# Optimization experiments

Hardware: AMD Instinct MI355X
Metric: run time of the kernel (lower is better)

Reference implementation:

```python
import jax, jax.numpy as jnp
import numpy as np

B, N, M, Q, H, D = 1, 512, 512, 128, 8, 16
CLIP = 10.0

def _xavier(key, shape):
    # xavier_uniform over last two dims (fan_in=Q, fan_out=D per head)
    fan_in, fan_out = shape[-2], shape[-1]
    limit = float(np.sqrt(6.0 / (fan_in + fan_out)))
    return jax.random.uniform(key, shape, jnp.float32, -limit, limit)

def setup_inputs() -> dict:
    key = jax.random.key(0)
    ks = jax.random.split(key, 12)
    return {
        "x": jax.random.normal(ks[0], (B, N, Q), jnp.float32),
        "y": jax.random.normal(ks[1], (B, M, Q), jnp.float32),
        "z": jax.random.normal(ks[2], (B, N, M, Q), jnp.float32),
        "mask": jax.random.randint(ks[3], (B, N, M), 0, 2, jnp.int32),
        "lambda_x": _xavier(ks[4], (H, Q, D)),
        "lambda_y": _xavier(ks[5], (H, Q, D)),
        "lambda_z1": _xavier(ks[6], (H, Q, D)),
        "lambda_z2": _xavier(ks[7], (H, Q, D)),
        "bias_lambda_x": jnp.zeros((H, D), jnp.float32),
        "bias_lambda_y": jnp.zeros((H, D), jnp.float32),
        "theta1": _xavier(ks[8], (H, Q, D)),
        "theta2": _xavier(ks[9], (H, Q, D)),
        "bias_theta": jnp.zeros((H, D), jnp.float32),
    }

def reference(x, y, z, mask, lambda_x, lambda_y, lambda_z1, lambda_z2,
              bias_lambda_x, bias_lambda_y, theta1, theta2, bias_theta):
    head_dim = lambda_x.shape[-1]
    # node projections: [B,N,H,D] / [B,M,H,D]
    r_x = jnp.einsum('bnq,hqd->bnhd', x, lambda_x) + bias_lambda_x
    r_y = jnp.einsum('bmq,hqd->bmhd', y, lambda_y) + bias_lambda_y
    # edge projections: [B,N,M,H,D]
    r_z1 = jnp.einsum('bnmq,hqd->bnmhd', z, lambda_z1)
    r_z2 = jnp.einsum('bnmq,hqd->bnmhd', z, lambda_z2)
    # broadcast-add node + edge terms, dot over D -> scores [B,H,N,M]
    att = jnp.einsum('bnmhd,bnmhd->bhnm',
                     r_x[:, :, None, :, :] + r_z1,
                     r_y[:, None, :, :, :] + r_z2)
    att = att * (head_dim ** -0.5)
    att = CLIP * jnp.tanh(att)
    att = jnp.where(mask[:, None, :, :] == 1, -jnp.inf, att)
    # NOTE: softmax over the N (source) axis, matching torch dim=-2
    w = jax.nn.softmax(att, axis=-2)
    x_p = jnp.einsum('bnq,hqd->bnhd', x, theta1)
    r = jnp.einsum('bhnm,bnhd->bmhd', w, x_p) + bias_theta
    return jnp.einsum('bmhd,hqd->bmq', r, theta2)
```

## Files before the change

### kernel.cpp

```cpp
#include <hip/hip_runtime.h>
#include <hip/hip_bf16.h>
#include <math.h>

typedef __attribute__((ext_vector_type(8))) short short8;
typedef __attribute__((ext_vector_type(4))) float f32x4;

#define NT 8

__global__ __launch_bounds__(128) void prep_kernel(
        const float* __restrict__ x,  const float* __restrict__ y,
        const float* __restrict__ lx, const float* __restrict__ ly,
        const float* __restrict__ t1,
        const float* __restrict__ lz1, const float* __restrict__ lz2,
        const float* __restrict__ th2, const float* __restrict__ bth,
        const float* __restrict__ blx, const float* __restrict__ bly,
        __hip_bfloat16* __restrict__ Wh, __hip_bfloat16* __restrict__ Wl,
        float* __restrict__ T2, float* __restrict__ ob,
        float* __restrict__ rx, float* __restrict__ ry, float* __restrict__ xp) {
    const int bid = blockIdx.x;
    const int t = threadIdx.x;
    if (bid < 256) {
        __shared__ float rows[4][128];
        const int role = bid >> 7;
        const int n0 = (bid & 127) * 4;
        const float* in = role ? y : x;
        const int o = t, h = o >> 4, d = o & 15;
#pragma unroll
        for (int j = 0; j < 4; ++j)
            rows[j][o] = in[(n0 + j) * 128 + o];
        __syncthreads();
        if (role == 0) {
            float a[4] = {0.f, 0.f, 0.f, 0.f}, b[4] = {0.f, 0.f, 0.f, 0.f};
#pragma unroll 4
            for (int q = 0; q < 128; ++q) {
                float wa = lx[(h * 128 + q) * 16 + d];
                float wb = t1[(h * 128 + q) * 16 + d];
#pragma unroll
                for (int j = 0; j < 4; ++j) {
                    a[j] = fmaf(rows[j][q], wa, a[j]);
                    b[j] = fmaf(rows[j][q], wb, b[j]);
                }
            }
            float bx = blx[o];
#pragma unroll
            for (int j = 0; j < 4; ++j) {
                rx[(n0 + j) * 128 + o] = a[j] + bx;
                xp[(n0 + j) * 128 + o] = b[j];
            }
        } else {
            float a[4] = {0.f, 0.f, 0.f, 0.f};
#pragma unroll 4
            for (int q = 0; q < 128; ++q) {
                float wa = ly[(h * 128 + q) * 16 + d];
#pragma unroll
                for (int j = 0; j < 4; ++j)
                    a[j] = fmaf(rows[j][q], wa, a[j]);
            }
            float by = bly[o];
#pragma unroll
            for (int j = 0; j < 4; ++j)
                ry[(n0 + j) * 128 + o] = a[j] + by;
        }
    } else {
        const int idx = (bid - 256) * 128 + t;
#pragma unroll
        for (int i = idx; i < 32768; i += 16384) {
            int op = i >> 7, q = i & 127;
            int h = op >> 5, wh = (op >> 4) & 1, d = op & 15;
            float v = (wh ? lz2 : lz1)[(h * 128 + q) * 16 + d];
            __hip_bfloat16 hb = __float2bfloat16(v);
            Wh[i] = hb;
            Wl[i] = __float2bfloat16(v - __bfloat162float(hb));
        }
        {
            int o = idx >> 7, q = idx & 127;
            int h = o >> 4, d = o & 15;
            T2[idx] = th2[(h * 128 + q) * 16 + d];
        }
        if (idx < 128) {
            int q = idx;
            float s = 0.f;
#pragma unroll
            for (int h = 0; h < 8; ++h)
#pragma unroll
                for (int c = 0; c < 4; ++c) {
                    float4 a = *(const float4*)&bth[h * 16 + c * 4];
                    float4 b = *(const float4*)&th2[(h * 128 + q) * 16 + c * 4];
                    s += a.x * b.x + a.y * b.y + a.z * b.z + a.w * b.w;
                }
            ob[q] = s;
        }
    }
}

__global__ __launch_bounds__(256) void big_kernel(
        const float* __restrict__ z,
        const int* __restrict__ mask,
        const __hip_bfloat16* __restrict__ Wh,
        const __hip_bfloat16* __restrict__ Wl,
        const float* __restrict__ rx,
        const float* __restrict__ ry,
        float* __restrict__ w) {
    __shared__ short zsh[2][64 * 128];
    __shared__ short zsl[2][64 * 128];
    const int m0 = blockIdx.x * 64;
    const int n0 = blockIdx.y * NT;
    const int tid = threadIdx.x;
    const int og = tid >> 6;
    const int l  = tid & 63;
    const int lg = l >> 4;
    const int lm = l & 15;

    const int srow = tid >> 2, kseg = tid & 3;
    const float* zbase = &z[(size_t)(m0 + srow) * 128 + kseg * 32];

    float4 ryr[2][4];
#pragma unroll
    for (int p = 0; p < 2; ++p)
#pragma unroll
        for (int i = 0; i < 4; ++i)
            ryr[p][i] = *(const float4*)&ry[(size_t)(m0 + i * 16 + lm) * 128 + (og * 2 + p) * 16 + lg * 4];

    float4 zr[8];
#define LOADZ(nn)                                                         \
    {                                                                     \
        const float* p_ = zbase + (size_t)(nn) * 65536;                   \
        _Pragma("unroll")                                                 \
        for (int c_ = 0; c_ < 8; ++c_) zr[c_] = *(const float4*)&p_[c_ * 4]; \
    }

#define CONVERT_WRITE(b)                                                  \
    {                                                                     \
        _Pragma("unroll")                                                 \
        for (int c8 = 0; c8 < 4; ++c8) {                                  \
            float vv[8] = {zr[2 * c8].x, zr[2 * c8].y, zr[2 * c8].z, zr[2 * c8].w, \
                           zr[2 * c8 + 1].x, zr[2 * c8 + 1].y, zr[2 * c8 + 1].z, zr[2 * c8 + 1].w}; \
            union { short8 s; __hip_bfloat16 h[8]; } uh, ul;              \
            _Pragma("unroll")                                             \
            for (int jj = 0; jj < 8; ++jj) {                              \
                float f_ = vv[jj];                                        \
                __hip_bfloat16 hb_ = __float2bfloat16(f_);                \
                uh.h[jj] = hb_;                                           \
                ul.h[jj] = __float2bfloat16(f_ - __bfloat162float(hb_));  \
            }                                                             \
            int cw_ = (kseg * 4 + c8) ^ (srow & 7);                       \
            *(short8*)&zsh[b][srow * 128 + cw_ * 8] = uh.s;               \
            *(short8*)&zsl[b][srow * 128 + cw_ * 8] = ul.s;               \
        }                                                                 \
    }

    LOADZ(n0);
    CONVERT_WRITE(0);
    LOADZ(n0 + 1);
    __syncthreads();

    for (int t = 0; t < NT; ++t) {
        const int n = n0 + t;
        const int cur = t & 1;
        const int mk = mask[n * 512 + m0 + l];

        f32x4 acc[4][4];
#pragma unroll
        for (int i = 0; i < 4; ++i)
#pragma unroll
            for (int pj = 0; pj < 4; ++pj) acc[i][pj] = (f32x4){0.f, 0.f, 0.f, 0.f};

#pragma unroll
        for (int ks = 0; ks < 4; ++ks) {
            short8 ah[4], al[4];
#pragma unroll
            for (int i = 0; i < 4; ++i) {
                int row = i * 16 + lm;
                int cw = (ks * 4 + lg) ^ (row & 7);
                ah[i] = *(const short8*)&zsh[cur][row * 128 + cw * 8];
                al[i] = *(const short8*)&zsl[cur][row * 128 + cw * 8];
            }
#pragma unroll
            for (int pj = 0; pj < 4; ++pj) {
                size_t off = (size_t)(og * 64 + pj * 16 + lm) * 128 + ks * 32 + lg * 8;
                short8 bh = *(const short8*)&Wh[off];
                short8 bl = *(const short8*)&Wl[off];
#pragma unroll
                for (int i = 0; i < 4; ++i) {
                    acc[i][pj] = __builtin_amdgcn_mfma_f32_16x16x32_bf16(bh, ah[i], acc[i][pj], 0, 0, 0);
                    acc[i][pj] = __builtin_amdgcn_mfma_f32_16x16x32_bf16(bh, al[i], acc[i][pj], 0, 0, 0);
                    acc[i][pj] = __builtin_amdgcn_mfma_f32_16x16x32_bf16(bl, ah[i], acc[i][pj], 0, 0, 0);
                }
            }
        }

#pragma unroll
        for (int p = 0; p < 2; ++p) {
            const int h = og * 2 + p;
            float4 rxt = *(const float4*)&rx[n * 128 + h * 16 + lg * 4];
            const float rxv[4] = {rxt.x, rxt.y, rxt.z, rxt.w};
            float t4[4];
#pragma unroll
            for (int i = 0; i < 4; ++i) {
                const float ryv[4] = {ryr[p][i].x, ryr[p][i].y, ryr[p][i].z, ryr[p][i].w};
                float s = 0.f;
#pragma unroll
                for (int r = 0; r < 4; ++r)
                    s = fmaf(rxv[r] + acc[i][p * 2][r], ryv[r] + acc[i][p * 2 + 1][r], s);
                s += __shfl_xor(s, 16);
                s += __shfl_xor(s, 32);
                t4[i] = s;
            }
            float ta = (lg & 1) ? t4[1] : t4[0];
            float tb = (lg & 1) ? t4[3] : t4[2];
            float s  = (lg & 2) ? tb : ta;
            float e1 = __expf(0.5f * s);
            float wv = __expf(-20.f / (e1 + 1.f));
            if (mk == 1) wv = 0.f;
            w[((size_t)(h * 512 + n)) * 512 + m0 + l] = wv;
        }

        if (t + 1 < NT) {
            CONVERT_WRITE(cur ^ 1);
            if (t + 2 < NT) LOADZ(n0 + t + 2);
        }
        __syncthreads();
    }
#undef LOADZ
#undef CONVERT_WRITE
}

__global__ __launch_bounds__(256) void finish_kernel(
        const float* __restrict__ w,
        const float* __restrict__ xp,
        const float* __restrict__ T2,
        const float* __restrict__ ob,
        float* __restrict__ out) {
    __shared__ float xps[512][16];
    __shared__ float red[32][8][16];
    __shared__ float ssum[32][8];
    __shared__ float rrs[8][128];
    const int m0 = blockIdx.x * 8;
    const int t  = threadIdx.x;
    const int ml = t & 7, g = t >> 3;

    for (int h = 0; h < 8; ++h) {
        for (int idx = t; idx < 512 * 4; idx += 256) {
            int nn = idx >> 2, c = idx & 3;
            *(float4*)&xps[nn][c * 4] = *(const float4*)&xp[nn * 128 + h * 16 + c * 4];
        }
        __syncthreads();

        const float* col = &w[((size_t)h * 512) * 512 + m0 + ml];
        float s = 0.f;
        float racc[16];
#pragma unroll
        for (int dd = 0; dd < 16; ++dd) racc[dd] = 0.f;
        for (int nn = g * 16; nn < g * 16 + 16; ++nn) {
            float e = col[(size_t)nn * 512];
            s += e;
#pragma unroll
            for (int c = 0; c < 4; ++c) {
                float4 xv = *(const float4*)&xps[nn][c * 4];
                racc[c * 4 + 0] = fmaf(e, xv.x, racc[c * 4 + 0]);
                racc[c * 4 + 1] = fmaf(e, xv.y, racc[c * 4 + 1]);
                racc[c * 4 + 2] = fmaf(e, xv.z, racc[c * 4 + 2]);
                racc[c * 4 + 3] = fmaf(e, xv.w, racc[c * 4 + 3]);
            }
        }
        ssum[g][ml] = s;
#pragma unroll
        for (int dd = 0; dd < 16; ++dd) red[g][ml][dd] = racc[dd];
        __syncthreads();

        if (t < 128) {
            const int m = t & 7, dd = t >> 3;
            float stot = 0.f;
#pragma unroll
            for (int gg = 0; gg < 32; ++gg) stot += ssum[gg][m];
            float v = 0.f;
#pragma unroll
            for (int gg = 0; gg < 32; ++gg) v += red[gg][m][dd];
            rrs[m][h * 16 + dd] = v / stot;
        }
        __syncthreads();
    }

    {
        const int q = t & 127, mg = t >> 7;
        float acc4[4] = {0.f, 0.f, 0.f, 0.f};
        for (int o4 = 0; o4 < 32; ++o4) {
            float tv[4];
#pragma unroll
            for (int k = 0; k < 4; ++k)
                tv[k] = T2[(o4 * 4 + k) * 128 + q];
#pragma unroll
            for (int j = 0; j < 4; ++j) {
                float4 rv = *(const float4*)&rrs[mg * 4 + j][o4 * 4];
                acc4[j] = fmaf(rv.x, tv[0], acc4[j]);
                acc4[j] = fmaf(rv.y, tv[1], acc4[j]);
                acc4[j] = fmaf(rv.z, tv[2], acc4[j]);
                acc4[j] = fmaf(rv.w, tv[3], acc4[j]);
            }
        }
        float b = ob[q];
#pragma unroll
        for (int j = 0; j < 4; ++j)
            out[(m0 + mg * 4 + j) * 128 + q] = acc4[j] + b;
    }
}

extern "C" void kernel_launch(void* const* d_in, const int* in_sizes, int n_in,
                              void* d_out, int out_size, void* d_ws, size_t ws_size,
                              hipStream_t stream) {
    (void)in_sizes; (void)n_in; (void)out_size; (void)ws_size;
    const float* x   = (const float*)d_in[0];
    const float* y   = (const float*)d_in[1];
    const float* z   = (const float*)d_in[2];
    const int*  mask = (const int*)d_in[3];
    const float* lx  = (const float*)d_in[4];
    const float* ly  = (const float*)d_in[5];
    const float* lz1 = (const float*)d_in[6];
    const float* lz2 = (const float*)d_in[7];
    const float* blx = (const float*)d_in[8];
    const float* bly = (const float*)d_in[9];
    const float* t1  = (const float*)d_in[10];
    const float* t2  = (const float*)d_in[11];
    const float* bth = (const float*)d_in[12];
    float* out = (float*)d_out;

    float* ws = (float*)d_ws;
    float* rx = ws;
    float* ry = rx + 65536;
    float* xp = ry + 65536;
    __hip_bfloat16* Wh = (__hip_bfloat16*)(xp + 65536);
    __hip_bfloat16* Wl = (__hip_bfloat16*)(xp + 65536 + 16384);
    float* T2  = xp + 65536 + 32768;
    float* ob  = T2 + 16384;
    float* wbuf= ob + 128;

    prep_kernel<<<dim3(384), dim3(128), 0, stream>>>(
        x, y, lx, ly, t1, lz1, lz2, t2, bth, blx, bly,
        Wh, Wl, T2, ob, rx, ry, xp);
    big_kernel<<<dim3(8, 64), dim3(256), 0, stream>>>(z, mask, Wh, Wl, rx, ry, wbuf);
    finish_kernel<<<dim3(64), dim3(256), 0, stream>>>(wbuf, xp, T2, ob, out);
}
```

Measured before the change: 297.7 us.

## Split finish kernel across heads and single-buffer z tile in big kernel

The finish stage, which looped over all 8 heads in 64 blocks, is split into a per-head pv_kernel launched on a 64x8 grid and a separate outg_kernel that applies the output projection. This raises parallelism in the tail stage, which was badly under-occupied. The big kernel's double-buffered LDS z tile becomes single-buffered, with a sync after the MFMA loop so the next tile's conversion overlaps the epilogue. That halves LDS use and may allow more resident blocks, at the cost of an extra barrier per iteration and an extra kernel launch.

```diff
diff --git a/kernel.cpp b/kernel.cpp
--- a/kernel.cpp
+++ b/kernel.cpp
@@ -101,8 +101,8 @@
         const float* __restrict__ rx,
         const float* __restrict__ ry,
         float* __restrict__ w) {
-    __shared__ short zsh[2][64 * 128];
-    __shared__ short zsl[2][64 * 128];
+    __shared__ short zsh[64 * 128];
+    __shared__ short zsl[64 * 128];
     const int m0 = blockIdx.x * 64;
     const int n0 = blockIdx.y * NT;
     const int tid = threadIdx.x;
@@ -129,7 +129,7 @@
         for (int c_ = 0; c_ < 8; ++c_) zr[c_] = *(const float4*)&p_[c_ * 4]; \
     }
 
-#define CONVERT_WRITE(b)                                                  \
+#define CONVERT_WRITE()                                                   \
     {                                                                     \
         _Pragma("unroll")                                                 \
         for (int c8 = 0; c8 < 4; ++c8) {                                  \
@@ -144,19 +144,18 @@
                 ul.h[jj] = __float2bfloat16(f_ - __bfloat162float(hb_));  \
             }                                                             \
             int cw_ = (kseg * 4 + c8) ^ (srow & 7);                       \
-            *(short8*)&zsh[b][srow * 128 + cw_ * 8] = uh.s;               \
-            *(short8*)&zsl[b][srow * 128 + cw_ * 8] = ul.s;               \
+            *(short8*)&zsh[srow * 128 + cw_ * 8] = uh.s;                  \
+            *(short8*)&zsl[srow * 128 + cw_ * 8] = ul.s;                  \
         }                                                                 \
     }
 
     LOADZ(n0);
-    CONVERT_WRITE(0);
+    CONVERT_WRITE();
     LOADZ(n0 + 1);
     __syncthreads();
 
     for (int t = 0; t < NT; ++t) {
         const int n = n0 + t;
-        const int cur = t & 1;
         const int mk = mask[n * 512 + m0 + l];
 
         f32x4 acc[4][4];
@@ -172,8 +171,8 @@
             for (int i = 0; i < 4; ++i) {
                 int row = i * 16 + lm;
                 int cw = (ks * 4 + lg) ^ (row & 7);
-                ah[i] = *(const short8*)&zsh[cur][row * 128 + cw * 8];
-                al[i] = *(const short8*)&zsl[cur][row * 128 + cw * 8];
+                ah[i] = *(const short8*)&zsh[row * 128 + cw * 8];
+                al[i] = *(const short8*)&zsl[row * 128 + cw * 8];
             }
 #pragma unroll
             for (int pj = 0; pj < 4; ++pj) {
@@ -187,6 +186,12 @@
                     acc[i][pj] = __builtin_amdgcn_mfma_f32_16x16x32_bf16(bl, ah[i], acc[i][pj], 0, 0, 0);
                 }
             }
+        }
+        __syncthreads();
+
+        if (t + 1 < NT) {
+            CONVERT_WRITE();
+            if (t + 2 < NT) LOADZ(n0 + t + 2);
         }
 
 #pragma unroll
@@ -215,94 +220,87 @@
             w[((size_t)(h * 512 + n)) * 512 + m0 + l] = wv;
         }
 
-        if (t + 1 < NT) {
-            CONVERT_WRITE(cur ^ 1);
-            if (t + 2 < NT) LOADZ(n0 + t + 2);
-        }
-        __syncthreads();
+        if (t + 1 < NT) __syncthreads();
     }
 #undef LOADZ
 #undef CONVERT_WRITE
 }
 
-__global__ __launch_bounds__(256) void finish_kernel(
+__global__ __launch_bounds__(256) void pv_kernel(
         const float* __restrict__ w,
         const float* __restrict__ xp,
-        const float* __restrict__ T2,
-        const float* __restrict__ ob,
-        float* __restrict__ out) {
-    __shared__ float xps[512][16];
-    __shared__ float red[32][8][16];
-    __shared__ float ssum[32][8];
-    __shared__ float rrs[8][128];
+        float* __restrict__ rr) {
+    __shared__ float red[32][8][17];
+    __shared__ float ssum[32][9];
     const int m0 = blockIdx.x * 8;
+    const int h  = blockIdx.y;
     const int t  = threadIdx.x;
     const int ml = t & 7, g = t >> 3;
 
-    for (int h = 0; h < 8; ++h) {
-        for (int idx = t; idx < 512 * 4; idx += 256) {
-            int nn = idx >> 2, c = idx & 3;
-            *(float4*)&xps[nn][c * 4] = *(const float4*)&xp[nn * 128 + h * 16 + c * 4];
-        }
-        __syncthreads();
-
-        const float* col = &w[((size_t)h * 512) * 512 + m0 + ml];
-        float s = 0.f;
-        float racc[16];
-#pragma unroll
-        for (int dd = 0; dd < 16; ++dd) racc[dd] = 0.f;
-        for (int nn = g * 16; nn < g * 16 + 16; ++nn) {
-            float e = col[(size_t)nn * 512];
-            s += e;
-#pragma unroll
-            for (int c = 0; c < 4; ++c) {
-                float4 xv = *(const float4*)&xps[nn][c * 4];
-                racc[c * 4 + 0] = fmaf(e, xv.x, racc[c * 4 + 0]);
-                racc[c * 4 + 1] = fmaf(e, xv.y, racc[c * 4 + 1]);
-                racc[c * 4 + 2] = fmaf(e, xv.z, racc[c * 4 + 2]);
-                racc[c * 4 + 3] = fmaf(e, xv.w, racc[c * 4 + 3]);
-            }
-        }
-        ssum[g][ml] = s;
-#pragma unroll
-        for (int dd = 0; dd < 16; ++dd) red[g][ml][dd] = racc[dd];
-        __syncthreads();
-
-        if (t < 128) {
-            const int m = t & 7, dd = t >> 3;
-            float stot = 0.f;
-#pragma unroll
-            for (int gg = 0; gg < 32; ++gg) stot += ssum[gg][m];
-            float v = 0.f;
-#pragma unroll
-            for (int gg = 0; gg < 32; ++gg) v += red[gg][m][dd];
-            rrs[m][h * 16 + dd] = v / stot;
-        }
-        __syncthreads();
-    }
-
-    {
-        const int q = t & 127, mg = t >> 7;
-        float acc4[4] = {0.f, 0.f, 0.f, 0.f};
-        for (int o4 = 0; o4 < 32; ++o4) {
-            float tv[4];
-#pragma unroll
-            for (int k = 0; k < 4; ++k)
-                tv[k] = T2[(o4 * 4 + k) * 128 + q];
-#pragma unroll
-            for (int j = 0; j < 4; ++j) {
-                float4 rv = *(const float4*)&rrs[mg * 4 + j][o4 * 4];
-                acc4[j] = fmaf(rv.x, tv[0], acc4[j]);
-                acc4[j] = fmaf(rv.y, tv[1], acc4[j]);
-                acc4[j] = fmaf(rv.z, tv[2], acc4[j]);
-                acc4[j] = fmaf(rv.w, tv[3], acc4[j]);
-            }
-        }
-        float b = ob[q];
+    const float* wcol = &w[(size_t)h * 262144 + m0 + ml];
+    const float* xph  = &xp[h * 16];
+
+    float racc[16];
+#pragma unroll
+    for (int dd = 0; dd < 16; ++dd) racc[dd] = 0.f;
+    float s = 0.f;
+    const int nnb = g * 16;
+#pragma unroll
+    for (int i = 0; i < 16; ++i) {
+        const int nn = nnb + i;
+        float e = wcol[(size_t)nn * 512];
+        s += e;
+        const float4* xr = (const float4*)&xph[nn * 128];
+        float4 x0 = xr[0], x1 = xr[1], x2 = xr[2], x3 = xr[3];
+        racc[0]  = fmaf(e, x0.x, racc[0]);  racc[1]  = fmaf(e, x0.y, racc[1]);
+        racc[2]  = fmaf(e, x0.z, racc[2]);  racc[3]  = fmaf(e, x0.w, racc[3]);
+        racc[4]  = fmaf(e, x1.x, racc[4]);  racc[5]  = fmaf(e, x1.y, racc[5]);
+        racc[6]  = fmaf(e, x1.z, racc[6]);  racc[7]  = fmaf(e, x1.w, racc[7]);
+        racc[8]  = fmaf(e, x2.x, racc[8]);  racc[9]  = fmaf(e, x2.y, racc[9]);
+        racc[10] = fmaf(e, x2.z, racc[10]); racc[11] = fmaf(e, x2.w, racc[11]);
+        racc[12] = fmaf(e, x3.x, racc[12]); racc[13] = fmaf(e, x3.y, racc[13]);
+        racc[14] = fmaf(e, x3.z, racc[14]); racc[15] = fmaf(e, x3.w, racc[15]);
+    }
+    ssum[g][ml] = s;
+#pragma unroll
+    for (int dd = 0; dd < 16; ++dd) red[g][ml][dd] = racc[dd];
+    __syncthreads();
+
+    if (t < 128) {
+        const int m = t & 7, dd = t >> 3;
+        float stot = 0.f;
+#pragma unroll
+        for (int gg = 0; gg < 32; ++gg) stot += ssum[gg][m];
+        float v = 0.f;
+#pragma unroll
+        for (int gg = 0; gg < 32; ++gg) v += red[gg][m][dd];
+        rr[(size_t)(m0 + m) * 128 + h * 16 + dd] = v / stot;
+    }
+}
+
+__global__ __launch_bounds__(128) void outg_kernel(const float* __restrict__ rr,
+                            const float* __restrict__ T2,
+                            const float* __restrict__ ob,
+                            float* __restrict__ out) {
+    __shared__ float rrow[4][128];
+    const int m0 = blockIdx.x * 4;
+    const int q = threadIdx.x;
+#pragma unroll
+    for (int j = 0; j < 4; ++j)
+        rrow[j][q] = rr[(m0 + j) * 128 + q];
+    __syncthreads();
+    float acc[4] = {0.f, 0.f, 0.f, 0.f};
+#pragma unroll 4
+    for (int o = 0; o < 128; ++o) {
+        float tv = T2[o * 128 + q];
 #pragma unroll
         for (int j = 0; j < 4; ++j)
-            out[(m0 + mg * 4 + j) * 128 + q] = acc4[j] + b;
-    }
+            acc[j] = fmaf(rrow[j][o], tv, acc[j]);
+    }
+    float b = ob[q];
+#pragma unroll
+    for (int j = 0; j < 4; ++j)
+        out[(m0 + j) * 128 + q] = acc[j] + b;
 }
 
 extern "C" void kernel_launch(void* const* d_in, const int* in_sizes, int n_in,
@@ -333,10 +331,12 @@
     float* T2  = xp + 65536 + 32768;
     float* ob  = T2 + 16384;
     float* wbuf= ob + 128;
+    float* rr  = wbuf + 2097152;
 
     prep_kernel<<<dim3(384), dim3(128), 0, stream>>>(
         x, y, lx, ly, t1, lz1, lz2, t2, bth, blx, bly,
         Wh, Wl, T2, ob, rx, ry, xp);
     big_kernel<<<dim3(8, 64), dim3(256), 0, stream>>>(z, mask, Wh, Wl, rx, ry, wbuf);
-    finish_kernel<<<dim3(64), dim3(256), 0, stream>>>(wbuf, xp, T2, ob, out);
-}
+    pv_kernel<<<dim3(64, 8), dim3(256), 0, stream>>>(wbuf, xp, rr);
+    outg_kernel<<<dim3(128), dim3(128), 0, stream>>>(rr, T2, ob, out);
+}
```

Result: no change. 299.4 us (+0.6%).
